# Optimization experiments

Hardware: AMD Instinct MI355X
Metric: run time of the kernel (lower is better)

The kernel has to match this reference:

```python
import jax, jax.numpy as jnp
import numpy as np

B, S, E = 2, 2048, 2048
H, G = 16, 4
HD = E // H          # 128
GD = HD * G          # 512
NGH = H // G         # 4 (tile factor for K/V heads)


def setup_inputs() -> dict:
    key = jax.random.key(0)
    ks = jax.random.split(key, 6)
    sc = 0.02
    return {
        "x": jax.random.normal(ks[0], (B, S, E), dtype=jnp.float32),
        "mask": jnp.ones((B, S, S), dtype=jnp.int32),
        "Wq": jax.random.normal(ks[1], (E, E), dtype=jnp.float32) * sc,
        "bq": jnp.zeros((E,), dtype=jnp.float32),
        "Wk": jax.random.normal(ks[2], (E, GD), dtype=jnp.float32) * sc,
        "bk": jnp.zeros((GD,), dtype=jnp.float32),
        "Wv": jax.random.normal(ks[3], (E, GD), dtype=jnp.float32) * sc,
        "bv": jnp.zeros((GD,), dtype=jnp.float32),
        "Wo": jax.random.normal(ks[4], (E, E), dtype=jnp.float32) * sc,
        "bo": jnp.zeros((E,), dtype=jnp.float32),
    }


def reference(x, mask, Wq, bq, Wk, bk, Wv, bv, Wo, bo):
    b, s, _ = x.shape
    # projections
    q = x @ Wq + bq                                   # [B,S,E]
    k = x @ Wk + bk                                   # [B,S,GD]
    v = x @ Wv + bv                                   # [B,S,GD]
    q = q.reshape(b, s, H, HD).transpose(0, 2, 1, 3)  # [B,H,S,hd]
    k = k.reshape(b, s, G, HD).transpose(0, 2, 1, 3)  # [B,G,S,hd]
    v = v.reshape(b, s, G, HD).transpose(0, 2, 1, 3)
    # torch .repeat(1, NGH, 1, 1): tile groups -> head h uses group h % G
    k = jnp.tile(k, (1, NGH, 1, 1))                   # [B,H,S,hd]
    v = jnp.tile(v, (1, NGH, 1, 1))
    scale = 1.0 / np.sqrt(HD).astype(np.float32)
    scores = jnp.einsum("bhqd,bhkd->bhqk", q, k) * scale
    m = mask[:, None, :, :]                           # [B,1,S,S]
    scores = jnp.where(m == 0, jnp.float32(-10000.0), scores)
    attn = jax.nn.softmax(scores, axis=-1)
    out = jnp.einsum("bhqk,bhkd->bhqd", attn, v)      # [B,H,S,hd]
    out = out.transpose(0, 2, 1, 3).reshape(b, s, E)  # [B,S,E]
    return out @ Wo + bo
```

## Files before the change

### kernel.cpp

```cpp
#include <hip/hip_runtime.h>

#define B_ 2
#define S_ 2048
#define E_ 2048
#define H_ 16
#define G_ 4
#define HD_ 128
#define GD_ 512
#define KVLD_ 1024
#define QKVN_ 3072
#define M_ (B_*S_)

using u16 = unsigned short;
using u32 = unsigned int;
typedef __attribute__((ext_vector_type(8))) short short8;
typedef __attribute__((ext_vector_type(4))) float f32x4;

#define QSCL 0.12751891114f
#define MASKED_L2 (-14427.0f)

__device__ __forceinline__ u16 f2bf(float f) {
  union { float f; unsigned u; } v; v.f = f;
  unsigned r = v.u + 0x7fff + ((v.u >> 16) & 1);
  return (u16)(r >> 16);
}

__device__ __forceinline__ void async16(const void* g, void* l) {
  __builtin_amdgcn_global_load_lds((const __attribute__((address_space(1))) unsigned int*)g,
                                   (__attribute__((address_space(3))) unsigned int*)l, 16, 0, 0);
}

__global__ __launch_bounds__(256) void cast_f32_bf16(const float* __restrict__ in,
                                                     u16* __restrict__ out, int n4) {
  int i = blockIdx.x * 256 + threadIdx.x;
  if (i >= n4) return;
  float4 v = ((const float4*)in)[i];
  union { u16 o[4]; uint2 u; } pk;
  pk.o[0] = f2bf(v.x); pk.o[1] = f2bf(v.y); pk.o[2] = f2bf(v.z); pk.o[3] = f2bf(v.w);
  *(uint2*)(out + (size_t)i * 4) = pk.u;
}

__global__ __launch_bounds__(256) void concat_bias3(const float* __restrict__ a,
                                                    const float* __restrict__ b,
                                                    const float* __restrict__ c,
                                                    float* __restrict__ o) {
  int t = blockIdx.x * 256 + threadIdx.x;
  if (t < 2048) o[t] = a[t];
  else if (t < 2560) o[t] = b[t - 2048];
  else if (t < 3072) o[t] = c[t - 2560];
}

__global__ __launch_bounds__(256) void transpose_cast(const float* __restrict__ W,
                                                      u16* __restrict__ Wt, int K, int N) {
  __shared__ u16 tile[64 * 72];
  int n0 = blockIdx.x * 64, k0 = blockIdx.y * 64;
  int t = threadIdx.x;
  int row = t >> 2;
  int seg = t & 3;
  const float* src = W + (size_t)(k0 + row) * N + n0 + seg * 16;
  #pragma unroll
  for (int i = 0; i < 4; ++i) {
    float4 v = *(const float4*)(src + i * 4);
    int nl = seg * 16 + i * 4;
    tile[(nl + 0) * 72 + row] = f2bf(v.x);
    tile[(nl + 1) * 72 + row] = f2bf(v.y);
    tile[(nl + 2) * 72 + row] = f2bf(v.z);
    tile[(nl + 3) * 72 + row] = f2bf(v.w);
  }
  __syncthreads();
  int nl = t >> 2, s2 = t & 3;
  u16* dst = Wt + (size_t)(n0 + nl) * K + k0 + s2 * 16;
  *(uint4*)dst       = *(const uint4*)&tile[nl * 72 + s2 * 16];
  *(uint4*)(dst + 8) = *(const uint4*)&tile[nl * 72 + s2 * 16 + 8];
}

__global__ __launch_bounds__(256) void transpose_v(const u16* __restrict__ KVb, u16* __restrict__ Vtg) {
  __shared__ u16 tile[64 * 72];
  int kv0 = blockIdx.x * 64;
  int gn0 = blockIdx.y * 64;
  int t = threadIdx.x;
  int row = t >> 2, seg = t & 3;
  int prow = (row & 15) * 4 + (row >> 4);
  const u16* src = KVb + (size_t)(kv0 + row) * KVLD_ + 512 + gn0 + seg * 16;
  union { uint4 v; u16 s[8]; } a, b;
  a.v = *(const uint4*)src; b.v = *(const uint4*)(src + 8);
  #pragma unroll
  for (int j = 0; j < 8; ++j) tile[(seg * 16 + j) * 72 + prow] = a.s[j];
  #pragma unroll
  for (int j = 0; j < 8; ++j) tile[(seg * 16 + 8 + j) * 72 + prow] = b.s[j];
  __syncthreads();
  int gl = t >> 2, ks2 = t & 3;
  int bb = kv0 >> 11;
  int s0 = kv0 & 2047;
  int gn = gn0 + gl;
  u16* dst = Vtg + (size_t)(bb * 512 + gn) * S_ + s0 + ks2 * 16;
  *(uint4*)dst       = *(const uint4*)&tile[gl * 72 + ks2 * 16];
  *(uint4*)(dst + 8) = *(const uint4*)&tile[gl * 72 + ks2 * 16 + 8];
}

__global__ __launch_bounds__(256) void mask_flags(const int* __restrict__ mask, int* __restrict__ flags) {
  int idx = blockIdx.x * 4 + (threadIdx.x >> 6);
  int lane = threadIdx.x & 63;
  int bb = idx >> 12, rg = (idx >> 5) & 127, kt = idx & 31;
  const int* base = mask + ((size_t)bb * S_ + rg * 16) * S_ + kt * 64;
  int row = lane >> 2, c0 = (lane & 3) * 16;
  int ok = 1;
  #pragma unroll
  for (int i = 0; i < 4; ++i) {
    int4 v = *(const int4*)&base[(size_t)row * S_ + c0 + i * 4];
    ok &= (v.x != 0) & (v.y != 0) & (v.z != 0) & (v.w != 0);
  }
  ok = __all(ok) ? 1 : 0;
  if (lane == 0) flags[idx] = ok;
}

__global__ __launch_bounds__(256) void gemm_qkv(const u16* __restrict__ A, const u16* __restrict__ Bt,
                                                const float* __restrict__ bias,
                                                u16* __restrict__ Qb, u16* __restrict__ KVb, int K) {
  __shared__ u16 As[128 * 32];
  __shared__ u16 Bs[128 * 32];
  int n0 = blockIdx.x * 128, m0 = blockIdx.y * 128;
  int t = threadIdx.x;
  int w = t >> 6, lane = t & 63, c = lane & 15, q = lane >> 4;
  int wm = w & 1, wn = w >> 1;
  int r0 = t >> 2, kc = t & 3;
  const u16* Ag0 = A  + (size_t)(m0 + r0) * K + kc * 8;
  const u16* Ag1 = A  + (size_t)(m0 + 64 + r0) * K + kc * 8;
  const u16* Bg0 = Bt + (size_t)(n0 + r0) * K + kc * 8;
  const u16* Bg1 = Bt + (size_t)(n0 + 64 + r0) * K + kc * 8;
  f32x4 acc[4][4] = {};
  for (int k0 = 0; k0 < K; k0 += 32) {
    async16(Ag0 + k0, &As[t * 8]);
    async16(Ag1 + k0, &As[2048 + t * 8]);
    async16(Bg0 + k0, &Bs[t * 8]);
    async16(Bg1 + k0, &Bs[2048 + t * 8]);
    __syncthreads();
    short8 af[4], bf[4];
    #pragma unroll
    for (int i = 0; i < 4; ++i) {
      af[i] = *(const short8*)&As[(wm * 64 + i * 16 + c) * 32 + q * 8];
      bf[i] = *(const short8*)&Bs[(wn * 64 + i * 16 + c) * 32 + q * 8];
    }
    #pragma unroll
    for (int i = 0; i < 4; ++i)
      #pragma unroll
      for (int j = 0; j < 4; ++j)
        acc[i][j] = __builtin_amdgcn_mfma_f32_16x16x32_bf16(af[i], bf[j], acc[i][j], 0, 0, 0);
    __syncthreads();
  }
  int isq = (n0 < 2048);
  #pragma unroll
  for (int i = 0; i < 4; ++i) {
    int mrow_base = m0 + wm * 64 + i * 16 + q * 4;
    #pragma unroll
    for (int j = 0; j < 4; ++j) {
      int coln = n0 + wn * 64 + j * 16 + c;
      float bv = bias[coln];
      #pragma unroll
      for (int r = 0; r < 4; ++r) {
        float v = acc[i][j][r] + bv;
        if (isq) Qb[(size_t)(mrow_base + r) * E_ + coln] = f2bf(v * QSCL);
        else     KVb[(size_t)(mrow_base + r) * KVLD_ + coln - 2048] = f2bf(v);
      }
    }
  }
}

__global__ __launch_bounds__(256) void gemm_k(const u16* __restrict__ A, const u16* __restrict__ Bt,
                                              const float* __restrict__ bias, float* __restrict__ Cout,
                                              int M, int N, int K) {
  __shared__ u16 As[128 * 32];
  __shared__ u16 Bs[128 * 32];
  int n0 = blockIdx.x * 128, m0 = blockIdx.y * 128;
  int t = threadIdx.x;
  int w = t >> 6, lane = t & 63, c = lane & 15, q = lane >> 4;
  int wm = w & 1, wn = w >> 1;
  int r0 = t >> 2, kc = t & 3;
  const u16* Ag0 = A  + (size_t)(m0 + r0) * K + kc * 8;
  const u16* Ag1 = A  + (size_t)(m0 + 64 + r0) * K + kc * 8;
  const u16* Bg0 = Bt + (size_t)(n0 + r0) * K + kc * 8;
  const u16* Bg1 = Bt + (size_t)(n0 + 64 + r0) * K + kc * 8;
  f32x4 acc[4][4] = {};
  for (int k0 = 0; k0 < K; k0 += 32) {
    async16(Ag0 + k0, &As[t * 8]);
    async16(Ag1 + k0, &As[2048 + t * 8]);
    async16(Bg0 + k0, &Bs[t * 8]);
    async16(Bg1 + k0, &Bs[2048 + t * 8]);
    __syncthreads();
    short8 af[4], bf[4];
    #pragma unroll
    for (int i = 0; i < 4; ++i) {
      af[i] = *(const short8*)&As[(wm * 64 + i * 16 + c) * 32 + q * 8];
      bf[i] = *(const short8*)&Bs[(wn * 64 + i * 16 + c) * 32 + q * 8];
    }
    #pragma unroll
    for (int i = 0; i < 4; ++i)
      #pragma unroll
      for (int j = 0; j < 4; ++j)
        acc[i][j] = __builtin_amdgcn_mfma_f32_16x16x32_bf16(af[i], bf[j], acc[i][j], 0, 0, 0);
    __syncthreads();
  }
  #pragma unroll
  for (int i = 0; i < 4; ++i) {
    int mrow_base = m0 + wm * 64 + i * 16 + q * 4;
    #pragma unroll
    for (int j = 0; j < 4; ++j) {
      int coln = n0 + wn * 64 + j * 16 + c;
      float bv = bias[coln];
      #pragma unroll
      for (int r = 0; r < 4; ++r)
        Cout[(size_t)(mrow_base + r) * N + coln] = acc[i][j][r] + bv;
    }
  }
}

__global__ __launch_bounds__(256) void attn_k(const u16* __restrict__ Q, const u16* __restrict__ KVb,
                                              const u16* __restrict__ Vtg, const int* __restrict__ mask,
                                              const int* __restrict__ mflags, u16* __restrict__ O) {
  __shared__ u16 Ks[2][64 * 128];
  __shared__ u16 Vs[2][128 * 64];
  __shared__ u16 Ps[4 * 32 * 64];
  int bid = blockIdx.x;
  int mt = bid & 15, h = (bid >> 4) & 15, bb = bid >> 8;
  int g = h & 3;
  int t = threadIdx.x, w = t >> 6, lane = t & 63, c = lane & 15, q = lane >> 4;
  int m0 = mt * 128;

  const u16* Qbase  = Q   + (size_t)(bb * S_ + m0) * E_ + h * HD_;
  const u16* Kbase  = KVb + (size_t)bb * S_ * KVLD_ + g * HD_;
  const u16* Vtbase = Vtg + (size_t)(bb * G_ + g) * HD_ * S_;

  int krow0 = t >> 4;
  int kkc   = ((t & 15) ^ (t >> 4)) * 8;
  const u16* Kst = Kbase + (size_t)krow0 * KVLD_ + kkc;
  int vn0 = t >> 3;
  int vkc = ((t & 7) ^ ((t >> 3) & 7)) * 8;
  const u16* Vst = Vtbase + (size_t)vn0 * S_ + vkc;

  int pwa[2][4], pra[2][2];
  #pragma unroll
  for (int s = 0; s < 2; ++s) {
    #pragma unroll
    for (int r = 0; r < 4; ++r) {
      int row = q * 4 + r;
      pwa[s][r] = w * 2048 + s * 1024 + row * 64 + (((c >> 1) ^ (row & 7)) * 8) + (c & 1) * 4;
    }
    #pragma unroll
    for (int ks = 0; ks < 2; ++ks)
      pra[s][ks] = w * 2048 + s * 1024 + c * 64 + (((ks * 4 + q) ^ (c & 7)) * 8);
  }

  short8 aq[2][4];
  #pragma unroll
  for (int s = 0; s < 2; ++s)
    #pragma unroll
    for (int k0 = 0; k0 < 4; ++k0)
      aq[s][k0] = *(const short8*)&Qbase[(size_t)(w * 32 + s * 16 + c) * E_ + k0 * 32 + q * 8];

  const short8 ones = {(short)0x3F80, (short)0x3F80, (short)0x3F80, (short)0x3F80,
                       (short)0x3F80, (short)0x3F80, (short)0x3F80, (short)0x3F80};

  f32x4 Oa[2][8] = {};
  f32x4 lacc[2] = {};

  #pragma unroll
  for (int p = 0; p < 4; ++p)
    async16(Kst + (size_t)(p * 16) * KVLD_, &Ks[0][p * 2048 + t * 8]);
  #pragma unroll
  for (int p = 0; p < 4; ++p)
    async16(Vst + (size_t)(p * 32) * S_, &Vs[0][p * 2048 + t * 8]);

  for (int kv0 = 0; kv0 < S_; kv0 += 64) {
    int cur = (kv0 >> 6) & 1;
    __syncthreads();
    if (kv0 + 64 < S_) {
      #pragma unroll
      for (int p = 0; p < 4; ++p)
        async16(Kst + (size_t)(kv0 + 64 + p * 16) * KVLD_, &Ks[cur ^ 1][p * 2048 + t * 8]);
      #pragma unroll
      for (int p = 0; p < 4; ++p)
        async16(Vst + (size_t)(p * 32) * S_ + kv0 + 64, &Vs[cur ^ 1][p * 2048 + t * 8]);
    }
    const u16* K_ = Ks[cur];
    const u16* V_ = Vs[cur];

    f32x4 sc[2][4] = {};
    #pragma unroll
    for (int k0 = 0; k0 < 4; ++k0) {
      short8 bk[4];
      #pragma unroll
      for (int ns = 0; ns < 4; ++ns)
        bk[ns] = *(const short8*)&K_[(ns * 16 + c) * 128 + (((k0 * 4 + q) ^ c) * 8)];
      #pragma unroll
      for (int s = 0; s < 2; ++s)
        #pragma unroll
        for (int ns = 0; ns < 4; ++ns)
          sc[s][ns] = __builtin_amdgcn_mfma_f32_16x16x32_bf16(aq[s][k0], bk[ns], sc[s][ns], 0, 0, 0);
    }
    #pragma unroll
    for (int s = 0; s < 2; ++s) {
      int flag = mflags[bb * 4096 + (mt * 8 + w * 2 + s) * 32 + (kv0 >> 6)];
      if (!flag) {
        #pragma unroll
        for (int r = 0; r < 4; ++r) {
          int qrow = m0 + w * 32 + s * 16 + q * 4 + r;
          const int* mrow = mask + ((size_t)bb * S_ + qrow) * S_ + kv0;
          #pragma unroll
          for (int ns = 0; ns < 4; ++ns)
            if (mrow[ns * 16 + c] == 0) sc[s][ns][r] = MASKED_L2;
        }
      }
    }
    #pragma unroll
    for (int s = 0; s < 2; ++s)
      #pragma unroll
      for (int r = 0; r < 4; ++r) {
        u32 u[4];
        #pragma unroll
        for (int ns = 0; ns < 4; ++ns) {
          float p = exp2f(sc[s][ns][r]);
          u[ns] = __float_as_uint(p) + 0x8000u;
        }
        uint2 pk;
        pk.x = __builtin_amdgcn_perm(u[1], u[0], 0x07060302);
        pk.y = __builtin_amdgcn_perm(u[3], u[2], 0x07060302);
        *(uint2*)&Ps[pwa[s][r]] = pk;
      }
    __asm__ volatile("" ::: "memory");
    #pragma unroll
    for (int ks = 0; ks < 2; ++ks) {
      short8 ap0 = *(const short8*)&Ps[pra[0][ks]];
      short8 ap1 = *(const short8*)&Ps[pra[1][ks]];
      lacc[0] = __builtin_amdgcn_mfma_f32_16x16x32_bf16(ap0, ones, lacc[0], 0, 0, 0);
      lacc[1] = __builtin_amdgcn_mfma_f32_16x16x32_bf16(ap1, ones, lacc[1], 0, 0, 0);
      #pragma unroll
      for (int d = 0; d < 8; ++d) {
        short8 bv = *(const short8*)&V_[(d * 16 + c) * 64 + (((ks * 4 + q) ^ (c & 7)) * 8)];
        Oa[0][d] = __builtin_amdgcn_mfma_f32_16x16x32_bf16(ap0, bv, Oa[0][d], 0, 0, 0);
        Oa[1][d] = __builtin_amdgcn_mfma_f32_16x16x32_bf16(ap1, bv, Oa[1][d], 0, 0, 0);
      }
    }
  }
  #pragma unroll
  for (int s = 0; s < 2; ++s) {
    float inv[4];
    #pragma unroll
    for (int r = 0; r < 4; ++r) inv[r] = 1.0f / lacc[s][r];
    #pragma unroll
    for (int d = 0; d < 8; ++d)
      #pragma unroll
      for (int r = 0; r < 4; ++r) {
        size_t off = (size_t)(bb * S_ + m0 + w * 32 + s * 16 + q * 4 + r) * E_ + h * HD_ + d * 16 + c;
        O[off] = f2bf(Oa[s][d][r] * inv[r]);
      }
  }
}

extern "C" void kernel_launch(void* const* d_in, const int* in_sizes, int n_in,
                              void* d_out, int out_size, void* d_ws, size_t ws_size,
                              hipStream_t stream) {
  const float* x    = (const float*)d_in[0];
  const int*   mask = (const int*)d_in[1];
  const float* Wq   = (const float*)d_in[2];
  const float* bq   = (const float*)d_in[3];
  const float* Wk   = (const float*)d_in[4];
  const float* bk   = (const float*)d_in[5];
  const float* Wv   = (const float*)d_in[6];
  const float* bv   = (const float*)d_in[7];
  const float* Wo   = (const float*)d_in[8];
  const float* bo   = (const float*)d_in[9];
  float* out = (float*)d_out;

  char* ws = (char*)d_ws;
  u16* xb    = (u16*)ws; ws += (size_t)M_ * E_ * 2;
  u16* Wqkvt = (u16*)ws; ws += (size_t)QKVN_ * E_ * 2;
  u16* Wot   = (u16*)ws; ws += (size_t)E_ * E_ * 2;
  u16* Qb    = (u16*)ws; ws += (size_t)M_ * E_ * 2;
  u16* KVb   = (u16*)ws; ws += (size_t)M_ * KVLD_ * 2;
  u16* Ob    = (u16*)ws; ws += (size_t)M_ * E_ * 2;
  u16* Vtg   = (u16*)ws; ws += (size_t)B_ * G_ * HD_ * S_ * 2;
  int* mfl   = (int*)ws; ws += (size_t)B_ * 128 * 32 * 4;
  float* bqkv = (float*)ws; ws += QKVN_ * 4;

  cast_f32_bf16<<<(M_ * E_ / 4 + 255) / 256, 256, 0, stream>>>(x, xb, M_ * E_ / 4);
  transpose_cast<<<dim3(E_ / 64,  E_ / 64), 256, 0, stream>>>(Wq, Wqkvt, E_, E_);
  transpose_cast<<<dim3(GD_ / 64, E_ / 64), 256, 0, stream>>>(Wk, Wqkvt + (size_t)2048 * E_, E_, GD_);
  transpose_cast<<<dim3(GD_ / 64, E_ / 64), 256, 0, stream>>>(Wv, Wqkvt + (size_t)2560 * E_, E_, GD_);
  transpose_cast<<<dim3(E_ / 64,  E_ / 64), 256, 0, stream>>>(Wo, Wot, E_, E_);
  concat_bias3<<<QKVN_ / 256, 256, 0, stream>>>(bq, bk, bv, bqkv);
  mask_flags<<<B_ * 128 * 32 / 4, 256, 0, stream>>>(mask, mfl);

  gemm_qkv<<<dim3(QKVN_ / 128, M_ / 128), 256, 0, stream>>>(xb, Wqkvt, bqkv, Qb, KVb, E_);
  transpose_v<<<dim3(M_ / 64, GD_ / 64), 256, 0, stream>>>(KVb, Vtg);

  attn_k<<<B_ * H_ * (S_ / 128), 256, 0, stream>>>(Qb, KVb, Vtg, mask, mfl, Ob);

  gemm_k<<<dim3(E_ / 128, M_ / 128), 256, 0, stream>>>(Ob, Wot, bo, out, M_, E_, E_);
}
```

Baseline: 389.0 us.

## Split attention work across eight waves and swizzle GEMM block order

The attention kernel now runs 512 threads per block, so each wave owns 16 query rows instead of 32. This halves per-wave accumulator registers and makes each thread issue half as many K/V tile loads. The GEMM kernels remap block indices in strided groups of eight to change the order in which output tiles are scheduled, aiming for better cache locality. exp2f is also replaced by the hardware exp2 builtin. The trade-offs are more waves competing for the same LDS K/V tiles, heavier barrier cost per block, and a swizzle that assumes the block count divides by eight.

```diff
diff --git a/kernel.cpp b/kernel.cpp
--- a/kernel.cpp
+++ b/kernel.cpp
@@ -119,7 +119,11 @@
                                                 u16* __restrict__ Qb, u16* __restrict__ KVb, int K) {
   __shared__ u16 As[128 * 32];
   __shared__ u16 Bs[128 * 32];
-  int n0 = blockIdx.x * 128, m0 = blockIdx.y * 128;
+  int nbx = gridDim.x;
+  int bid = blockIdx.y * nbx + blockIdx.x;
+  int chunk = (nbx * gridDim.y) >> 3;
+  int swz = (bid & 7) * chunk + (bid >> 3);
+  int n0 = (swz % nbx) * 128, m0 = (swz / nbx) * 128;
   int t = threadIdx.x;
   int w = t >> 6, lane = t & 63, c = lane & 15, q = lane >> 4;
   int wm = w & 1, wn = w >> 1;
@@ -171,7 +175,11 @@
                                               int M, int N, int K) {
   __shared__ u16 As[128 * 32];
   __shared__ u16 Bs[128 * 32];
-  int n0 = blockIdx.x * 128, m0 = blockIdx.y * 128;
+  int nbx = gridDim.x;
+  int bid = blockIdx.y * nbx + blockIdx.x;
+  int chunk = (nbx * gridDim.y) >> 3;
+  int swz = (bid & 7) * chunk + (bid >> 3);
+  int n0 = (swz % nbx) * 128, m0 = (swz / nbx) * 128;
   int t = threadIdx.x;
   int w = t >> 6, lane = t & 63, c = lane & 15, q = lane >> 4;
   int wm = w & 1, wn = w >> 1;
@@ -214,12 +222,12 @@
   }
 }
 
-__global__ __launch_bounds__(256) void attn_k(const u16* __restrict__ Q, const u16* __restrict__ KVb,
+__global__ __launch_bounds__(512) void attn_k(const u16* __restrict__ Q, const u16* __restrict__ KVb,
                                               const u16* __restrict__ Vtg, const int* __restrict__ mask,
                                               const int* __restrict__ mflags, u16* __restrict__ O) {
   __shared__ u16 Ks[2][64 * 128];
   __shared__ u16 Vs[2][128 * 64];
-  __shared__ u16 Ps[4 * 32 * 64];
+  __shared__ u16 Ps[8 * 16 * 64];
   int bid = blockIdx.x;
   int mt = bid & 15, h = (bid >> 4) & 15, bb = bid >> 8;
   int g = h & 3;
@@ -231,60 +239,55 @@
   const u16* Vtbase = Vtg + (size_t)(bb * G_ + g) * HD_ * S_;
 
   int krow0 = t >> 4;
-  int kkc   = ((t & 15) ^ (t >> 4)) * 8;
+  int kkc   = ((t & 15) ^ (krow0 & 15)) * 8;
   const u16* Kst = Kbase + (size_t)krow0 * KVLD_ + kkc;
   int vn0 = t >> 3;
-  int vkc = ((t & 7) ^ ((t >> 3) & 7)) * 8;
+  int vkc = ((t & 7) ^ (vn0 & 7)) * 8;
   const u16* Vst = Vtbase + (size_t)vn0 * S_ + vkc;
 
-  int pwa[2][4], pra[2][2];
-  #pragma unroll
-  for (int s = 0; s < 2; ++s) {
-    #pragma unroll
-    for (int r = 0; r < 4; ++r) {
-      int row = q * 4 + r;
-      pwa[s][r] = w * 2048 + s * 1024 + row * 64 + (((c >> 1) ^ (row & 7)) * 8) + (c & 1) * 4;
-    }
-    #pragma unroll
-    for (int ks = 0; ks < 2; ++ks)
-      pra[s][ks] = w * 2048 + s * 1024 + c * 64 + (((ks * 4 + q) ^ (c & 7)) * 8);
-  }
-
-  short8 aq[2][4];
-  #pragma unroll
-  for (int s = 0; s < 2; ++s)
-    #pragma unroll
-    for (int k0 = 0; k0 < 4; ++k0)
-      aq[s][k0] = *(const short8*)&Qbase[(size_t)(w * 32 + s * 16 + c) * E_ + k0 * 32 + q * 8];
+  int pwa[4], pra[2];
+  #pragma unroll
+  for (int r = 0; r < 4; ++r) {
+    int row = q * 4 + r;
+    pwa[r] = w * 1024 + row * 64 + (((c >> 1) ^ (row & 7)) * 8) + (c & 1) * 4;
+  }
+  #pragma unroll
+  for (int ks = 0; ks < 2; ++ks)
+    pra[ks] = w * 1024 + c * 64 + (((ks * 4 + q) ^ (c & 7)) * 8);
+
+  short8 aq[4];
+  #pragma unroll
+  for (int k0 = 0; k0 < 4; ++k0)
+    aq[k0] = *(const short8*)&Qbase[(size_t)(w * 16 + c) * E_ + k0 * 32 + q * 8];
 
   const short8 ones = {(short)0x3F80, (short)0x3F80, (short)0x3F80, (short)0x3F80,
                        (short)0x3F80, (short)0x3F80, (short)0x3F80, (short)0x3F80};
 
-  f32x4 Oa[2][8] = {};
-  f32x4 lacc[2] = {};
-
-  #pragma unroll
-  for (int p = 0; p < 4; ++p)
-    async16(Kst + (size_t)(p * 16) * KVLD_, &Ks[0][p * 2048 + t * 8]);
-  #pragma unroll
-  for (int p = 0; p < 4; ++p)
-    async16(Vst + (size_t)(p * 32) * S_, &Vs[0][p * 2048 + t * 8]);
+  f32x4 Oa[8] = {};
+  f32x4 lacc = {};
+
+  #pragma unroll
+  for (int p = 0; p < 2; ++p)
+    async16(Kst + (size_t)(p * 32) * KVLD_, &Ks[0][p * 4096 + t * 8]);
+  #pragma unroll
+  for (int p = 0; p < 2; ++p)
+    async16(Vst + (size_t)(p * 64) * S_, &Vs[0][p * 4096 + t * 8]);
 
   for (int kv0 = 0; kv0 < S_; kv0 += 64) {
     int cur = (kv0 >> 6) & 1;
     __syncthreads();
     if (kv0 + 64 < S_) {
       #pragma unroll
-      for (int p = 0; p < 4; ++p)
-        async16(Kst + (size_t)(kv0 + 64 + p * 16) * KVLD_, &Ks[cur ^ 1][p * 2048 + t * 8]);
-      #pragma unroll
-      for (int p = 0; p < 4; ++p)
-        async16(Vst + (size_t)(p * 32) * S_ + kv0 + 64, &Vs[cur ^ 1][p * 2048 + t * 8]);
+      for (int p = 0; p < 2; ++p)
+        async16(Kst + (size_t)(kv0 + 64 + p * 32) * KVLD_, &Ks[cur ^ 1][p * 4096 + t * 8]);
+      #pragma unroll
+      for (int p = 0; p < 2; ++p)
+        async16(Vst + (size_t)(p * 64) * S_ + kv0 + 64, &Vs[cur ^ 1][p * 4096 + t * 8]);
     }
     const u16* K_ = Ks[cur];
     const u16* V_ = Vs[cur];
 
-    f32x4 sc[2][4] = {};
+    f32x4 sc[4] = {};
     #pragma unroll
     for (int k0 = 0; k0 < 4; ++k0) {
       short8 bk[4];
@@ -292,66 +295,57 @@
       for (int ns = 0; ns < 4; ++ns)
         bk[ns] = *(const short8*)&K_[(ns * 16 + c) * 128 + (((k0 * 4 + q) ^ c) * 8)];
       #pragma unroll
-      for (int s = 0; s < 2; ++s)
-        #pragma unroll
-        for (int ns = 0; ns < 4; ++ns)
-          sc[s][ns] = __builtin_amdgcn_mfma_f32_16x16x32_bf16(aq[s][k0], bk[ns], sc[s][ns], 0, 0, 0);
-    }
-    #pragma unroll
-    for (int s = 0; s < 2; ++s) {
-      int flag = mflags[bb * 4096 + (mt * 8 + w * 2 + s) * 32 + (kv0 >> 6)];
+      for (int ns = 0; ns < 4; ++ns)
+        sc[ns] = __builtin_amdgcn_mfma_f32_16x16x32_bf16(aq[k0], bk[ns], sc[ns], 0, 0, 0);
+    }
+    {
+      int flag = mflags[bb * 4096 + (mt * 8 + w) * 32 + (kv0 >> 6)];
       if (!flag) {
         #pragma unroll
         for (int r = 0; r < 4; ++r) {
-          int qrow = m0 + w * 32 + s * 16 + q * 4 + r;
+          int qrow = m0 + w * 16 + q * 4 + r;
           const int* mrow = mask + ((size_t)bb * S_ + qrow) * S_ + kv0;
           #pragma unroll
           for (int ns = 0; ns < 4; ++ns)
-            if (mrow[ns * 16 + c] == 0) sc[s][ns][r] = MASKED_L2;
+            if (mrow[ns * 16 + c] == 0) sc[ns][r] = MASKED_L2;
         }
       }
     }
     #pragma unroll
-    for (int s = 0; s < 2; ++s)
-      #pragma unroll
-      for (int r = 0; r < 4; ++r) {
-        u32 u[4];
-        #pragma unroll
-        for (int ns = 0; ns < 4; ++ns) {
-          float p = exp2f(sc[s][ns][r]);
-          u[ns] = __float_as_uint(p) + 0x8000u;
-        }
-        uint2 pk;
-        pk.x = __builtin_amdgcn_perm(u[1], u[0], 0x07060302);
-        pk.y = __builtin_amdgcn_perm(u[3], u[2], 0x07060302);
-        *(uint2*)&Ps[pwa[s][r]] = pk;
-      }
+    for (int r = 0; r < 4; ++r) {
+      u32 u[4];
+      #pragma unroll
+      for (int ns = 0; ns < 4; ++ns) {
+        float p = __builtin_amdgcn_exp2f(sc[ns][r]);
+        u[ns] = __float_as_uint(p) + 0x8000u;
+      }
+      uint2 pk;
+      pk.x = __builtin_amdgcn_perm(u[1], u[0], 0x07060302);
+      pk.y = __builtin_amdgcn_perm(u[3], u[2], 0x07060302);
+      *(uint2*)&Ps[pwa[r]] = pk;
+    }
     __asm__ volatile("" ::: "memory");
     #pragma unroll
     for (int ks = 0; ks < 2; ++ks) {
-      short8 ap0 = *(const short8*)&Ps[pra[0][ks]];
-      short8 ap1 = *(const short8*)&Ps[pra[1][ks]];
-      lacc[0] = __builtin_amdgcn_mfma_f32_16x16x32_bf16(ap0, ones, lacc[0], 0, 0, 0);
-      lacc[1] = __builtin_amdgcn_mfma_f32_16x16x32_bf16(ap1, ones, lacc[1], 0, 0, 0);
+      short8 ap = *(const short8*)&Ps[pra[ks]];
+      lacc = __builtin_amdgcn_mfma_f32_16x16x32_bf16(ap, ones, lacc, 0, 0, 0);
       #pragma unroll
       for (int d = 0; d < 8; ++d) {
         short8 bv = *(const short8*)&V_[(d * 16 + c) * 64 + (((ks * 4 + q) ^ (c & 7)) * 8)];
-        Oa[0][d] = __builtin_amdgcn_mfma_f32_16x16x32_bf16(ap0, bv, Oa[0][d], 0, 0, 0);
-        Oa[1][d] = __builtin_amdgcn_mfma_f32_16x16x32_bf16(ap1, bv, Oa[1][d], 0, 0, 0);
-      }
-    }
-  }
-  #pragma unroll
-  for (int s = 0; s < 2; ++s) {
+        Oa[d] = __builtin_amdgcn_mfma_f32_16x16x32_bf16(ap, bv, Oa[d], 0, 0, 0);
+      }
+    }
+  }
+  {
     float inv[4];
     #pragma unroll
-    for (int r = 0; r < 4; ++r) inv[r] = 1.0f / lacc[s][r];
+    for (int r = 0; r < 4; ++r) inv[r] = 1.0f / lacc[r];
     #pragma unroll
     for (int d = 0; d < 8; ++d)
       #pragma unroll
       for (int r = 0; r < 4; ++r) {
-        size_t off = (size_t)(bb * S_ + m0 + w * 32 + s * 16 + q * 4 + r) * E_ + h * HD_ + d * 16 + c;
-        O[off] = f2bf(Oa[s][d][r] * inv[r]);
+        size_t off = (size_t)(bb * S_ + m0 + w * 16 + q * 4 + r) * E_ + h * HD_ + d * 16 + c;
+        O[off] = f2bf(Oa[d][r] * inv[r]);
       }
   }
 }
@@ -393,7 +387,7 @@
   gemm_qkv<<<dim3(QKVN_ / 128, M_ / 128), 256, 0, stream>>>(xb, Wqkvt, bqkv, Qb, KVb, E_);
   transpose_v<<<dim3(M_ / 64, GD_ / 64), 256, 0, stream>>>(KVb, Vtg);
 
-  attn_k<<<B_ * H_ * (S_ / 128), 256, 0, stream>>>(Qb, KVb, Vtg, mask, mfl, Ob);
+  attn_k<<<B_ * H_ * (S_ / 128), 512, 0, stream>>>(Qb, KVb, Vtg, mask, mfl, Ob);
 
   gemm_k<<<dim3(E_ / 128, M_ / 128), 256, 0, stream>>>(Ob, Wot, bo, out, M_, E_, E_);
 }
```

New measurement: 362.8 us. 1.07x faster.
